# Performance work log

Hardware: AMD Instinct MI355X
Metric: run time of the kernel (lower is better)

The kernel has to match this reference:

```python
import jax, jax.numpy as jnp
import numpy as np

N_NODES = 100_000
N_EDGES = 1_250_000
N_GRAPHS = 2048


def gcn_conv(x, src, dst, norm, W, b, n):
    # PyG GCNConv: x' = D^-1/2 (A+I) D^-1/2 (x W) + b  (self-loops already in src/dst)
    h = x @ W                                   # [N, 64]
    msg = h[src] * norm[:, None]                # [E+N, 64] gather + scale
    out = jax.ops.segment_sum(msg, dst, num_segments=n)  # scatter-add
    return out + b


def build_norm(edge_index, n):
    # add self loops, compute symmetric gcn normalization
    loop = jnp.arange(n, dtype=edge_index.dtype)
    src = jnp.concatenate([edge_index[0], loop])
    dst = jnp.concatenate([edge_index[1], loop])
    deg = jax.ops.segment_sum(jnp.ones_like(dst, dtype=jnp.float32), dst, num_segments=n)
    dinv = jnp.where(deg > 0, jax.lax.rsqrt(deg), 0.0)
    norm = dinv[src] * dinv[dst]
    return src, dst, norm


def setup_inputs() -> dict:
    key = jax.random.key(0)
    ks = jax.random.split(key, 11)
    return {
        "x": jax.random.randint(ks[0], (N_NODES,), 0, 28, dtype=jnp.int32),
        "edge_index": jax.random.randint(ks[1], (2, N_EDGES), 0, N_NODES, dtype=jnp.int32),
        "edge_attr": jax.random.randint(ks[2], (N_EDGES,), 0, 4, dtype=jnp.int32),
        "batch": jnp.sort(jax.random.randint(ks[3], (N_NODES,), 0, N_GRAPHS, dtype=jnp.int32)),
        "emb_table": jax.random.normal(ks[4], (28, 64), dtype=jnp.float32),
        "W1": jax.random.normal(ks[5], (64, 64), dtype=jnp.float32) * 0.125,
        "b1": jax.random.normal(ks[6], (64,), dtype=jnp.float32) * 0.02,
        "W2": jax.random.normal(ks[7], (64, 64), dtype=jnp.float32) * 0.125,
        "b2": jax.random.normal(ks[8], (64,), dtype=jnp.float32) * 0.02,
        "lin_W": jax.random.normal(ks[9], (64, 1), dtype=jnp.float32) * 0.125,
        "lin_b": jax.random.normal(ks[10], (1,), dtype=jnp.float32) * 0.02,
    }


def reference(x, edge_index, edge_attr, batch, emb_table, W1, b1, W2, b2, lin_W, lin_b):
    n = x.shape[0]
    src, dst, norm = build_norm(edge_index, n)
    h = emb_table[x]                                   # node embedding lookup [N, 64]
    h = jax.nn.relu(gcn_conv(h, src, dst, norm, W1, b1, n))
    # dropout is identity at inference (training=False)
    emb = gcn_conv(h, src, dst, norm, W2, b2, n)        # [N, 64]
    y = emb @ lin_W + lin_b                              # [N, 1]
    out = jax.ops.segment_sum(y, batch, num_segments=N_GRAPHS)  # graph readout
    return out.squeeze(-1)                               # [N_GRAPHS]
```

## Files before the change

kernel.cpp:

```cpp
#include <hip/hip_runtime.h>

#define N_CLS 28
#define DIM   64
#define VB    128
#define VB_SH 7
#define SLK   32
#define NBKT_S 800
#define PT_T  512
#define IPT   12
#define PTILE (PT_T * IPT)
#define STG   9280

__global__ void __launch_bounds__(PT_T)
k_part(const int* __restrict__ src, const int* __restrict__ dst,
       int* __restrict__ ebkt,
       const float* __restrict__ emb, const float* __restrict__ W1,
       const float* __restrict__ W2, const float* __restrict__ linW,
       const float* __restrict__ b2, const float* __restrict__ linb,
       float* __restrict__ T1g, float* __restrict__ ug, float* __restrict__ ccg,
       float* __restrict__ out,
       int E, int nbkt, int nblk, int out_size) {
    int tid = threadIdx.x, b = blockIdx.x;
    if (b == nblk) {
        int lane = tid & 63, wv = tid >> 6;
        for (int r = wv; r < N_CLS; r += PT_T / 64) {
            float acc = 0.f;
#pragma unroll
            for (int k = 0; k < DIM; ++k) acc += emb[r * DIM + k] * W1[k * DIM + lane];
            T1g[r * DIM + lane] = acc;
        }
        if (wv == 0) {
            float acc = 0.f;
#pragma unroll
            for (int k = 0; k < DIM; ++k) acc += W2[lane * DIM + k] * linW[k];
            ug[lane] = acc;
        }
        if (tid == 0) {
            float s = 0.f;
            for (int k = 0; k < DIM; ++k) s += b2[k] * linW[k];
            ccg[0] = s + linb[0];
        }
        for (int i = tid; i < out_size; i += PT_T) out[i] = 0.f;
        return;
    }
    __shared__ int h[NBKT_S];
    __shared__ int offs[NBKT_S];
    __shared__ int wt[8];
    __shared__ int seg0tot;
    __shared__ __align__(16) int stage[STG];
    for (int i = tid; i < nbkt; i += PT_T) h[i] = 0;
    __syncthreads();
    int s0 = b * PTILE;
    int pk[IPT], ar[IPT];
#pragma unroll
    for (int g = 0; g < IPT / 4; ++g) {
        int i4 = s0 + (g * PT_T + tid) * 4;
        if (i4 + 3 < E) {
            int4 sv = *(const int4*)&src[i4];
            int4 dv = *(const int4*)&dst[i4];
            int ss[4] = {sv.x, sv.y, sv.z, sv.w};
            int dd[4] = {dv.x, dv.y, dv.z, dv.w};
#pragma unroll
            for (int j = 0; j < 4; ++j) {
                int bkt = dd[j] >> VB_SH;
                int r = atomicAdd(&h[bkt], 1);
                pk[g * 4 + j] = ss[j] | ((dd[j] & (VB - 1)) << 17);
                ar[g * 4 + j] = bkt | (r << 10);
            }
        } else {
#pragma unroll
            for (int j = 0; j < 4; ++j) {
                int idx = i4 + j;
                ar[g * 4 + j] = -1;
                if (idx < E) {
                    int s = src[idx], d = dst[idx];
                    int bkt = d >> VB_SH;
                    int r = atomicAdd(&h[bkt], 1);
                    pk[g * 4 + j] = s | ((d & (VB - 1)) << 17);
                    ar[g * 4 + j] = bkt | (r << 10);
                }
            }
        }
    }
    __syncthreads();
    int lane = tid & 63, wave = tid >> 6;
    {
        int w0 = (tid < nbkt) ? ((min(h[tid], SLK - 1) + 4) & ~3) : 0;
        int incl = w0;
#pragma unroll
        for (int o = 1; o < 64; o <<= 1) {
            int n = __shfl_up(incl, o);
            if (lane >= o) incl += n;
        }
        if (lane == 63) wt[wave] = incl;
        __syncthreads();
        int woff = 0, tot = 0;
#pragma unroll
        for (int w2 = 0; w2 < 8; ++w2) { int t2 = wt[w2]; woff += (w2 < wave) ? t2 : 0; tot += t2; }
        if (tid < nbkt) offs[tid] = woff + incl - w0;
        if (tid == 0) seg0tot = tot;
        __syncthreads();
    }
    {
        int i1 = tid + 512;
        int w1 = (i1 < nbkt) ? ((min(h[i1], SLK - 1) + 4) & ~3) : 0;
        int incl = w1;
#pragma unroll
        for (int o = 1; o < 64; o <<= 1) {
            int n = __shfl_up(incl, o);
            if (lane >= o) incl += n;
        }
        if (lane == 63) wt[wave] = incl;
        __syncthreads();
        int woff = 0;
#pragma unroll
        for (int w2 = 0; w2 < 8; ++w2) woff += (w2 < wave) ? wt[w2] : 0;
        if (i1 < nbkt) offs[i1] = seg0tot + woff + incl - w1;
        __syncthreads();
    }
    for (int i = tid; i < nbkt; i += PT_T) stage[offs[i]] = min(h[i], SLK - 1);
#pragma unroll
    for (int k = 0; k < IPT; ++k) {
        int a = ar[k];
        if (a >= 0) {
            int bkt = a & 1023, r = a >> 10;
            if (r < SLK - 1) stage[offs[bkt] + 1 + r] = pk[k];
        }
    }
    __syncthreads();
    for (int i = tid; i < nbkt; i += PT_T) {
        int c = min(h[i], SLK - 1);
        int nq = (c + 4) >> 2;
        int4* gq = (int4*)(ebkt + ((size_t)i * nblk + b) * SLK);
        const int4* sq = (const int4*)&stage[offs[i]];
        for (int q = 0; q < nq; ++q) gq[q] = sq[q];
    }
}

#define RUN_FOREACH_J(rv, jj, BODY)                                      \
    {                                                                    \
        int4 q0 = (rv)[0];                                               \
        int c = q0.x;                                                    \
        int e3[3] = {q0.y, q0.z, q0.w};                                  \
        _Pragma("unroll")                                                \
        for (int j_ = 0; j_ < 3; ++j_)                                   \
            if (j_ < c && (j_ & 1) == (jj)) { int p = e3[j_]; BODY; }    \
        for (int base = 3; base < c; base += 4) {                        \
            int4 q = (rv)[(base + 1) >> 2];                              \
            int e4[4] = {q.x, q.y, q.z, q.w};                            \
            _Pragma("unroll")                                            \
            for (int j_ = 0; j_ < 4; ++j_)                               \
                if (base + j_ < c && ((base + j_) & 1) == (jj))          \
                    { int p = e4[j_]; BODY; }                            \
        }                                                                \
    }

__device__ __forceinline__ float wsum64(float q) {
    q += __int_as_float(__builtin_amdgcn_update_dpp(0, __float_as_int(q), 0x111, 0xf, 0xf, true));
    q += __int_as_float(__builtin_amdgcn_update_dpp(0, __float_as_int(q), 0x112, 0xf, 0xf, true));
    q += __int_as_float(__builtin_amdgcn_update_dpp(0, __float_as_int(q), 0x114, 0xf, 0xf, true));
    q += __int_as_float(__builtin_amdgcn_update_dpp(0, __float_as_int(q), 0x118, 0xf, 0xf, true));
    q += __int_as_float(__builtin_amdgcn_update_dpp(0, __float_as_int(q), 0x142, 0xa, 0xf, false));
    q += __int_as_float(__builtin_amdgcn_update_dpp(0, __float_as_int(q), 0x143, 0xc, 0xf, false));
    return q;
}

__global__ void __launch_bounds__(512)
k_deg(const int* __restrict__ ebkt, const int* __restrict__ x,
      float2* __restrict__ xd, int N, int nblk) {
    __shared__ int dg[VB];
    int tid = threadIdx.x, k = blockIdx.x;
    if (tid < VB) dg[tid] = 0;
    __syncthreads();
    int rid = tid >> 1, j = tid & 1;
    if (rid < nblk) {
        const int4* rv = (const int4*)(ebkt + ((size_t)k * nblk + rid) * SLK);
        RUN_FOREACH_J(rv, j, atomicAdd(&dg[p >> 17], 1));
    }
    __syncthreads();
    int v = k * VB + tid;
    if (tid < VB && v < N)
        xd[v] = make_float2(rsqrtf((float)(dg[tid] + 1)), __int_as_float(x[v]));
}

__global__ void __launch_bounds__(512)
k_l1(const int* __restrict__ ebkt, const float2* __restrict__ xd,
     const float* __restrict__ T1, const float* __restrict__ b1,
     const float* __restrict__ u, float* __restrict__ t, int N, int nblk) {
    __shared__ __align__(16) float cnt[VB * N_CLS];
    __shared__ float T1s[N_CLS * DIM];
    __shared__ float b1s[DIM], us[DIM];
    int tid = threadIdx.x, b = blockIdx.x;
    for (int i = tid; i < VB * N_CLS; i += 512) cnt[i] = 0.f;
    for (int i = tid; i < N_CLS * DIM; i += 512) T1s[i] = T1[i];
    if (tid < DIM) { b1s[tid] = b1[tid]; us[tid] = u[tid]; }
    __syncthreads();
    int rid = tid >> 1, j = tid & 1;
    if (rid < nblk) {
        const int4* rv = (const int4*)(ebkt + ((size_t)b * nblk + rid) * SLK);
        RUN_FOREACH_J(rv, j, {
            float2 xs = xd[p & 0x1FFFF];
            atomicAdd(&cnt[(p >> 17) * N_CLS + __float_as_int(xs.y)], xs.x);
        });
    }
    __syncthreads();
    int wave = tid >> 6, lane = tid & 63;
    float tc[N_CLS];
#pragma unroll
    for (int c = 0; c < N_CLS; ++c) tc[c] = T1s[c * DIM + lane];
    float b1l = b1s[lane], ul = us[lane];
    int v0 = b * VB;
    for (int it = 0; it < 16; ++it) {
        int lv = wave * 16 + it;
        int v = v0 + lv;
        if (v >= N) break;
        float2 pv = xd[v];
        float dv = pv.x;
        int xv = __float_as_int(pv.y);
        const float4* row = (const float4*)&cnt[lv * N_CLS];
        float acc = dv * T1s[xv * DIM + lane];
#pragma unroll
        for (int q4 = 0; q4 < 7; ++q4) {
            float4 r = row[q4];
            acc += r.x * tc[q4 * 4 + 0] + r.y * tc[q4 * 4 + 1]
                 + r.z * tc[q4 * 4 + 2] + r.w * tc[q4 * 4 + 3];
        }
        float hh = fmaxf(dv * acc + b1l, 0.f);
        float q = wsum64(hh * ul);
        if (lane == 63) t[v] = dv * q;
    }
}

__global__ void __launch_bounds__(512)
k_l2(const int* __restrict__ ebkt, const float2* __restrict__ xd,
     const float* __restrict__ t, const float* __restrict__ cc,
     const int* __restrict__ batch, float* __restrict__ out,
     int N, int n_graphs, int nblk) {
    __shared__ float acc[VB];
    __shared__ float og[64];
    __shared__ int g0s;
    int tid = threadIdx.x, k = blockIdx.x;
    if (tid < VB) acc[tid] = 0.f;
    if (tid < 64) og[tid] = 0.f;
    if (tid == 0) g0s = batch[min(k * VB, N - 1)];
    __syncthreads();
    int rid = tid >> 1, j = tid & 1;
    if (rid < nblk) {
        const int4* rv = (const int4*)(ebkt + ((size_t)k * nblk + rid) * SLK);
        RUN_FOREACH_J(rv, j, atomicAdd(&acc[p >> 17], t[p & 0x1FFFF]));
    }
    __syncthreads();
    int v = k * VB + tid;
    if (tid < VB && v < N) {
        float y = xd[v].x * (acc[tid] + t[v]) + cc[0];
        int g = batch[v];
        int off = g - g0s;
        if (off < 64) atomicAdd(&og[off], y);
        else atomicAdd(&out[g], y);
    }
    __syncthreads();
    if (tid < 64) {
        float val = og[tid];
        int g = g0s + tid;
        if (val != 0.f && g < n_graphs) atomicAdd(&out[g], val);
    }
}

extern "C" void kernel_launch(void* const* d_in, const int* in_sizes, int n_in,
                              void* d_out, int out_size, void* d_ws, size_t ws_size,
                              hipStream_t stream) {
    const int*   x     = (const int*)d_in[0];
    const int*   ei    = (const int*)d_in[1];
    const int*   batch = (const int*)d_in[3];
    const float* emb   = (const float*)d_in[4];
    const float* W1    = (const float*)d_in[5];
    const float* b1    = (const float*)d_in[6];
    const float* W2    = (const float*)d_in[7];
    const float* b2    = (const float*)d_in[8];
    const float* linW  = (const float*)d_in[9];
    const float* linb  = (const float*)d_in[10];

    const int N = in_sizes[0];
    const int E = in_sizes[1] / 2;
    const int* srcp = ei;
    const int* dstp = ei + E;
    float* out = (float*)d_out;

    const int nbkt = (N + VB - 1) >> VB_SH;
    const int nblk = (E + PTILE - 1) / PTILE;

    char* w = (char*)d_ws;
    float2* xd   = (float2*)w; w += (size_t)N * 8;
    float*  t    = (float*)w;  w += (size_t)N * 4;
    int*    ebkt = (int*)w;    w += (size_t)nbkt * nblk * SLK * 4;
    float*  T1   = (float*)w;  w += (size_t)N_CLS * DIM * 4;
    float*  u    = (float*)w;  w += DIM * 4;
    float*  cc   = (float*)w;  w += 16;

    k_part<<<nblk + 1, PT_T, 0, stream>>>(srcp, dstp, ebkt,
                                          emb, W1, W2, linW, b2, linb,
                                          T1, u, cc, out, E, nbkt, nblk, out_size);
    k_deg <<<nbkt, 512, 0, stream>>>(ebkt, x, xd, N, nblk);
    k_l1  <<<nbkt, 512, 0, stream>>>(ebkt, xd, T1, b1, u, t, N, nblk);
    k_l2  <<<nbkt, 512, 0, stream>>>(ebkt, xd, t, cc, batch, out, N, out_size, nblk);
}
```

Baseline: 62.92 us.

## Write partitioned edge buckets contiguously per block with separate offset/count table

The partition kernel now copies its whole shared-memory stage as one contiguous, coalesced stream per block instead of writing each bucket into a fixed 32-slot padded region. It also writes a packed offset/count word per (block, bucket) into a separate table. The consumer kernels read that table to find their slice, then scan it without the inline count header. This cuts padded global writes and scattered small stores, at the cost of an extra dependent load for the offset word in each consumer thread.

After: 66.79 us. 1.06x slower.

```diff
diff --git a/kernel.cpp b/kernel.cpp
--- a/kernel.cpp
+++ b/kernel.cpp
@@ -4,7 +4,7 @@
 #define DIM   64
 #define VB    128
 #define VB_SH 7
-#define SLK   32
+#define CMAX  31
 #define NBKT_S 800
 #define PT_T  512
 #define IPT   12
@@ -13,7 +13,7 @@
 
 __global__ void __launch_bounds__(PT_T)
 k_part(const int* __restrict__ src, const int* __restrict__ dst,
-       int* __restrict__ ebkt,
+       int* __restrict__ ebkt, int* __restrict__ offcnt,
        const float* __restrict__ emb, const float* __restrict__ W1,
        const float* __restrict__ W2, const float* __restrict__ linW,
        const float* __restrict__ b2, const float* __restrict__ linb,
@@ -46,7 +46,7 @@
     __shared__ int h[NBKT_S];
     __shared__ int offs[NBKT_S];
     __shared__ int wt[8];
-    __shared__ int seg0tot;
+    __shared__ int seg0tot, seg1tot;
     __shared__ __align__(16) int stage[STG];
     for (int i = tid; i < nbkt; i += PT_T) h[i] = 0;
     __syncthreads();
@@ -85,7 +85,7 @@
     __syncthreads();
     int lane = tid & 63, wave = tid >> 6;
     {
-        int w0 = (tid < nbkt) ? ((min(h[tid], SLK - 1) + 4) & ~3) : 0;
+        int w0 = (tid < nbkt) ? ((min(h[tid], CMAX) + 3) & ~3) : 0;
         int incl = w0;
 #pragma unroll
         for (int o = 1; o < 64; o <<= 1) {
@@ -103,7 +103,7 @@
     }
     {
         int i1 = tid + 512;
-        int w1 = (i1 < nbkt) ? ((min(h[i1], SLK - 1) + 4) & ~3) : 0;
+        int w1 = (i1 < nbkt) ? ((min(h[i1], CMAX) + 3) & ~3) : 0;
         int incl = w1;
 #pragma unroll
         for (int o = 1; o < 64; o <<= 1) {
@@ -112,47 +112,38 @@
         }
         if (lane == 63) wt[wave] = incl;
         __syncthreads();
-        int woff = 0;
-#pragma unroll
-        for (int w2 = 0; w2 < 8; ++w2) woff += (w2 < wave) ? wt[w2] : 0;
+        int woff = 0, tot = 0;
+#pragma unroll
+        for (int w2 = 0; w2 < 8; ++w2) { int t2 = wt[w2]; woff += (w2 < wave) ? t2 : 0; tot += t2; }
         if (i1 < nbkt) offs[i1] = seg0tot + woff + incl - w1;
+        if (tid == 0) seg1tot = tot;
         __syncthreads();
     }
-    for (int i = tid; i < nbkt; i += PT_T) stage[offs[i]] = min(h[i], SLK - 1);
+    for (int i = tid; i < nbkt; i += PT_T)
+        offcnt[(size_t)b * nbkt + i] = offs[i] | (min(h[i], CMAX) << 16);
 #pragma unroll
     for (int k = 0; k < IPT; ++k) {
         int a = ar[k];
         if (a >= 0) {
             int bkt = a & 1023, r = a >> 10;
-            if (r < SLK - 1) stage[offs[bkt] + 1 + r] = pk[k];
-        }
-    }
-    __syncthreads();
-    for (int i = tid; i < nbkt; i += PT_T) {
-        int c = min(h[i], SLK - 1);
-        int nq = (c + 4) >> 2;
-        int4* gq = (int4*)(ebkt + ((size_t)i * nblk + b) * SLK);
-        const int4* sq = (const int4*)&stage[offs[i]];
-        for (int q = 0; q < nq; ++q) gq[q] = sq[q];
-    }
-}
-
-#define RUN_FOREACH_J(rv, jj, BODY)                                      \
-    {                                                                    \
-        int4 q0 = (rv)[0];                                               \
-        int c = q0.x;                                                    \
-        int e3[3] = {q0.y, q0.z, q0.w};                                  \
+            if (r < CMAX) stage[offs[bkt] + r] = pk[k];
+        }
+    }
+    __syncthreads();
+    int total4 = (seg0tot + seg1tot) >> 2;
+    int4* gq = (int4*)(ebkt + (size_t)b * STG);
+    const int4* sq = (const int4*)stage;
+    for (int q = tid; q < total4; q += PT_T) gq[q] = sq[q];
+}
+
+#define RUN_FOREACH_J(rv, c, jj, BODY)                                   \
+    for (int base_ = 0; base_ < (c); base_ += 4) {                       \
+        int4 q_ = (rv)[base_ >> 2];                                      \
+        int e4_[4] = {q_.x, q_.y, q_.z, q_.w};                           \
         _Pragma("unroll")                                                \
-        for (int j_ = 0; j_ < 3; ++j_)                                   \
-            if (j_ < c && (j_ & 1) == (jj)) { int p = e3[j_]; BODY; }    \
-        for (int base = 3; base < c; base += 4) {                        \
-            int4 q = (rv)[(base + 1) >> 2];                              \
-            int e4[4] = {q.x, q.y, q.z, q.w};                            \
-            _Pragma("unroll")                                            \
-            for (int j_ = 0; j_ < 4; ++j_)                               \
-                if (base + j_ < c && ((base + j_) & 1) == (jj))          \
-                    { int p = e4[j_]; BODY; }                            \
-        }                                                                \
+        for (int j_ = 0; j_ < 4; ++j_)                                   \
+            if (base_ + j_ < (c) && ((base_ + j_) & 1) == (jj))          \
+                { int p = e4_[j_]; BODY; }                               \
     }
 
 __device__ __forceinline__ float wsum64(float q) {
@@ -166,16 +157,19 @@
 }
 
 __global__ void __launch_bounds__(512)
-k_deg(const int* __restrict__ ebkt, const int* __restrict__ x,
-      float2* __restrict__ xd, int N, int nblk) {
+k_deg(const int* __restrict__ ebkt, const int* __restrict__ offcnt,
+      const int* __restrict__ x, float2* __restrict__ xd,
+      int N, int nbkt, int nblk) {
     __shared__ int dg[VB];
     int tid = threadIdx.x, k = blockIdx.x;
     if (tid < VB) dg[tid] = 0;
     __syncthreads();
     int rid = tid >> 1, j = tid & 1;
     if (rid < nblk) {
-        const int4* rv = (const int4*)(ebkt + ((size_t)k * nblk + rid) * SLK);
-        RUN_FOREACH_J(rv, j, atomicAdd(&dg[p >> 17], 1));
+        int oc = offcnt[(size_t)rid * nbkt + k];
+        int c = oc >> 16, off = oc & 0xFFFF;
+        const int4* rv = (const int4*)(ebkt + (size_t)rid * STG + off);
+        RUN_FOREACH_J(rv, c, j, atomicAdd(&dg[p >> 17], 1));
     }
     __syncthreads();
     int v = k * VB + tid;
@@ -184,9 +178,10 @@
 }
 
 __global__ void __launch_bounds__(512)
-k_l1(const int* __restrict__ ebkt, const float2* __restrict__ xd,
-     const float* __restrict__ T1, const float* __restrict__ b1,
-     const float* __restrict__ u, float* __restrict__ t, int N, int nblk) {
+k_l1(const int* __restrict__ ebkt, const int* __restrict__ offcnt,
+     const float2* __restrict__ xd, const float* __restrict__ T1,
+     const float* __restrict__ b1, const float* __restrict__ u,
+     float* __restrict__ t, int N, int nbkt, int nblk) {
     __shared__ __align__(16) float cnt[VB * N_CLS];
     __shared__ float T1s[N_CLS * DIM];
     __shared__ float b1s[DIM], us[DIM];
@@ -197,8 +192,10 @@
     __syncthreads();
     int rid = tid >> 1, j = tid & 1;
     if (rid < nblk) {
-        const int4* rv = (const int4*)(ebkt + ((size_t)b * nblk + rid) * SLK);
-        RUN_FOREACH_J(rv, j, {
+        int oc = offcnt[(size_t)rid * nbkt + b];
+        int c = oc >> 16, off = oc & 0xFFFF;
+        const int4* rv = (const int4*)(ebkt + (size_t)rid * STG + off);
+        RUN_FOREACH_J(rv, c, j, {
             float2 xs = xd[p & 0x1FFFF];
             atomicAdd(&cnt[(p >> 17) * N_CLS + __float_as_int(xs.y)], xs.x);
         });
@@ -232,10 +229,10 @@
 }
 
 __global__ void __launch_bounds__(512)
-k_l2(const int* __restrict__ ebkt, const float2* __restrict__ xd,
-     const float* __restrict__ t, const float* __restrict__ cc,
-     const int* __restrict__ batch, float* __restrict__ out,
-     int N, int n_graphs, int nblk) {
+k_l2(const int* __restrict__ ebkt, const int* __restrict__ offcnt,
+     const float2* __restrict__ xd, const float* __restrict__ t,
+     const float* __restrict__ cc, const int* __restrict__ batch,
+     float* __restrict__ out, int N, int n_graphs, int nbkt, int nblk) {
     __shared__ float acc[VB];
     __shared__ float og[64];
     __shared__ int g0s;
@@ -246,8 +243,10 @@
     __syncthreads();
     int rid = tid >> 1, j = tid & 1;
     if (rid < nblk) {
-        const int4* rv = (const int4*)(ebkt + ((size_t)k * nblk + rid) * SLK);
-        RUN_FOREACH_J(rv, j, atomicAdd(&acc[p >> 17], t[p & 0x1FFFF]));
+        int oc = offcnt[(size_t)rid * nbkt + k];
+        int c = oc >> 16, off = oc & 0xFFFF;
+        const int4* rv = (const int4*)(ebkt + (size_t)rid * STG + off);
+        RUN_FOREACH_J(rv, c, j, atomicAdd(&acc[p >> 17], t[p & 0x1FFFF]));
     }
     __syncthreads();
     int v = k * VB + tid;
@@ -290,17 +289,18 @@
     const int nblk = (E + PTILE - 1) / PTILE;
 
     char* w = (char*)d_ws;
-    float2* xd   = (float2*)w; w += (size_t)N * 8;
-    float*  t    = (float*)w;  w += (size_t)N * 4;
-    int*    ebkt = (int*)w;    w += (size_t)nbkt * nblk * SLK * 4;
-    float*  T1   = (float*)w;  w += (size_t)N_CLS * DIM * 4;
-    float*  u    = (float*)w;  w += DIM * 4;
-    float*  cc   = (float*)w;  w += 16;
-
-    k_part<<<nblk + 1, PT_T, 0, stream>>>(srcp, dstp, ebkt,
+    float2* xd     = (float2*)w; w += (size_t)N * 8;
+    float*  t      = (float*)w;  w += (size_t)N * 4;
+    int*    ebkt   = (int*)w;    w += (size_t)nblk * STG * 4;
+    int*    offcnt = (int*)w;    w += (size_t)nblk * nbkt * 4;
+    float*  T1     = (float*)w;  w += (size_t)N_CLS * DIM * 4;
+    float*  u      = (float*)w;  w += DIM * 4;
+    float*  cc     = (float*)w;  w += 16;
+
+    k_part<<<nblk + 1, PT_T, 0, stream>>>(srcp, dstp, ebkt, offcnt,
                                           emb, W1, W2, linW, b2, linb,
                                           T1, u, cc, out, E, nbkt, nblk, out_size);
-    k_deg <<<nbkt, 512, 0, stream>>>(ebkt, x, xd, N, nblk);
-    k_l1  <<<nbkt, 512, 0, stream>>>(ebkt, xd, T1, b1, u, t, N, nblk);
-    k_l2  <<<nbkt, 512, 0, stream>>>(ebkt, xd, t, cc, batch, out, N, out_size, nblk);
-}
+    k_deg <<<nbkt, 512, 0, stream>>>(ebkt, offcnt, x, xd, N, nbkt, nblk);
+    k_l1  <<<nbkt, 512, 0, stream>>>(ebkt, offcnt, xd, T1, b1, u, t, N, nbkt, nblk);
+    k_l2  <<<nbkt, 512, 0, stream>>>(ebkt, offcnt, xd, t, cc, batch, out, N, out_size, nbkt, nblk);
+}
```

## Shrink partition tiles and slots, assign one thread per edge run

Applied to the files above, without the earlier changes.

The partition kernel now runs 256 threads per block with 8 edges per thread. That gives many more, smaller partition blocks, and the per-bucket slot shrinks from 32 to 20 ints to match, which cuts LDS staging and should raise occupancy. The two fixed-size scan passes become a loop over 256-wide segments with a running carry. The degree and layer consumer kernels drop the two-threads-per-run split and loop one thread per run, because there are now more, shorter runs. The risks are a larger run count per bucket for consumers to walk, uneven work when the run count exceeds 512, and a tighter 19-edge cap per slot.

Measured after the change: 74.18 us. 1.18x slower.

```diff
diff --git a/kernel.cpp b/kernel.cpp
--- a/kernel.cpp
+++ b/kernel.cpp
@@ -4,12 +4,13 @@
 #define DIM   64
 #define VB    128
 #define VB_SH 7
-#define SLK   32
+#define SLK   20
+#define CMAX  (SLK - 1)
 #define NBKT_S 800
-#define PT_T  512
-#define IPT   12
+#define PT_T  256
+#define IPT   8
 #define PTILE (PT_T * IPT)
-#define STG   9280
+#define STG   4400
 
 __global__ void __launch_bounds__(PT_T)
 k_part(const int* __restrict__ src, const int* __restrict__ dst,
@@ -45,8 +46,7 @@
     }
     __shared__ int h[NBKT_S];
     __shared__ int offs[NBKT_S];
-    __shared__ int wt[8];
-    __shared__ int seg0tot;
+    __shared__ int wt[4];
     __shared__ __align__(16) int stage[STG];
     for (int i = tid; i < nbkt; i += PT_T) h[i] = 0;
     __syncthreads();
@@ -84,9 +84,11 @@
     }
     __syncthreads();
     int lane = tid & 63, wave = tid >> 6;
-    {
-        int w0 = (tid < nbkt) ? ((min(h[tid], SLK - 1) + 4) & ~3) : 0;
-        int incl = w0;
+    int carry = 0;
+    for (int seg = 0; seg < nbkt; seg += PT_T) {
+        int i = seg + tid;
+        int w = (i < nbkt) ? ((min(h[i], CMAX) + 4) & ~3) : 0;
+        int incl = w;
 #pragma unroll
         for (int o = 1; o < 64; o <<= 1) {
             int n = __shfl_up(incl, o);
@@ -96,40 +98,27 @@
         __syncthreads();
         int woff = 0, tot = 0;
 #pragma unroll
-        for (int w2 = 0; w2 < 8; ++w2) { int t2 = wt[w2]; woff += (w2 < wave) ? t2 : 0; tot += t2; }
-        if (tid < nbkt) offs[tid] = woff + incl - w0;
-        if (tid == 0) seg0tot = tot;
+        for (int w2 = 0; w2 < 4; ++w2) {
+            int t2 = wt[w2];
+            woff += (w2 < wave) ? t2 : 0;
+            tot += t2;
+        }
+        if (i < nbkt) offs[i] = carry + woff + incl - w;
+        carry += tot;
         __syncthreads();
     }
-    {
-        int i1 = tid + 512;
-        int w1 = (i1 < nbkt) ? ((min(h[i1], SLK - 1) + 4) & ~3) : 0;
-        int incl = w1;
-#pragma unroll
-        for (int o = 1; o < 64; o <<= 1) {
-            int n = __shfl_up(incl, o);
-            if (lane >= o) incl += n;
-        }
-        if (lane == 63) wt[wave] = incl;
-        __syncthreads();
-        int woff = 0;
-#pragma unroll
-        for (int w2 = 0; w2 < 8; ++w2) woff += (w2 < wave) ? wt[w2] : 0;
-        if (i1 < nbkt) offs[i1] = seg0tot + woff + incl - w1;
-        __syncthreads();
-    }
-    for (int i = tid; i < nbkt; i += PT_T) stage[offs[i]] = min(h[i], SLK - 1);
+    for (int i = tid; i < nbkt; i += PT_T) stage[offs[i]] = min(h[i], CMAX);
 #pragma unroll
     for (int k = 0; k < IPT; ++k) {
         int a = ar[k];
         if (a >= 0) {
             int bkt = a & 1023, r = a >> 10;
-            if (r < SLK - 1) stage[offs[bkt] + 1 + r] = pk[k];
+            if (r < CMAX) stage[offs[bkt] + 1 + r] = pk[k];
         }
     }
     __syncthreads();
     for (int i = tid; i < nbkt; i += PT_T) {
-        int c = min(h[i], SLK - 1);
+        int c = min(h[i], CMAX);
         int nq = (c + 4) >> 2;
         int4* gq = (int4*)(ebkt + ((size_t)i * nblk + b) * SLK);
         const int4* sq = (const int4*)&stage[offs[i]];
@@ -137,21 +126,20 @@
     }
 }
 
-#define RUN_FOREACH_J(rv, jj, BODY)                                      \
+#define RUN_FOREACH(rv, BODY)                                            \
     {                                                                    \
         int4 q0 = (rv)[0];                                               \
         int c = q0.x;                                                    \
         int e3[3] = {q0.y, q0.z, q0.w};                                  \
         _Pragma("unroll")                                                \
         for (int j_ = 0; j_ < 3; ++j_)                                   \
-            if (j_ < c && (j_ & 1) == (jj)) { int p = e3[j_]; BODY; }    \
-        for (int base = 3; base < c; base += 4) {                        \
-            int4 q = (rv)[(base + 1) >> 2];                              \
-            int e4[4] = {q.x, q.y, q.z, q.w};                            \
+            if (j_ < c) { int p = e3[j_]; BODY; }                        \
+        for (int base_ = 3; base_ < c; base_ += 4) {                     \
+            int4 q_ = (rv)[(base_ + 1) >> 2];                            \
+            int e4_[4] = {q_.x, q_.y, q_.z, q_.w};                       \
             _Pragma("unroll")                                            \
             for (int j_ = 0; j_ < 4; ++j_)                               \
-                if (base + j_ < c && ((base + j_) & 1) == (jj))          \
-                    { int p = e4[j_]; BODY; }                            \
+                if (base_ + j_ < c) { int p = e4_[j_]; BODY; }           \
         }                                                                \
     }
 
@@ -172,10 +160,9 @@
     int tid = threadIdx.x, k = blockIdx.x;
     if (tid < VB) dg[tid] = 0;
     __syncthreads();
-    int rid = tid >> 1, j = tid & 1;
-    if (rid < nblk) {
+    for (int rid = tid; rid < nblk; rid += 512) {
         const int4* rv = (const int4*)(ebkt + ((size_t)k * nblk + rid) * SLK);
-        RUN_FOREACH_J(rv, j, atomicAdd(&dg[p >> 17], 1));
+        RUN_FOREACH(rv, atomicAdd(&dg[p >> 17], 1));
     }
     __syncthreads();
     int v = k * VB + tid;
@@ -195,10 +182,9 @@
     for (int i = tid; i < N_CLS * DIM; i += 512) T1s[i] = T1[i];
     if (tid < DIM) { b1s[tid] = b1[tid]; us[tid] = u[tid]; }
     __syncthreads();
-    int rid = tid >> 1, j = tid & 1;
-    if (rid < nblk) {
+    for (int rid = tid; rid < nblk; rid += 512) {
         const int4* rv = (const int4*)(ebkt + ((size_t)b * nblk + rid) * SLK);
-        RUN_FOREACH_J(rv, j, {
+        RUN_FOREACH(rv, {
             float2 xs = xd[p & 0x1FFFF];
             atomicAdd(&cnt[(p >> 17) * N_CLS + __float_as_int(xs.y)], xs.x);
         });
@@ -244,10 +230,9 @@
     if (tid < 64) og[tid] = 0.f;
     if (tid == 0) g0s = batch[min(k * VB, N - 1)];
     __syncthreads();
-    int rid = tid >> 1, j = tid & 1;
-    if (rid < nblk) {
+    for (int rid = tid; rid < nblk; rid += 512) {
         const int4* rv = (const int4*)(ebkt + ((size_t)k * nblk + rid) * SLK);
-        RUN_FOREACH_J(rv, j, atomicAdd(&acc[p >> 17], t[p & 0x1FFFF]));
+        RUN_FOREACH(rv, atomicAdd(&acc[p >> 17], t[p & 0x1FFFF]));
     }
     __syncthreads();
     int v = k * VB + tid;
```
